# Optimization experiments

Hardware: AMD Instinct MI355X
Metric: run time of the kernel (lower is better)

The kernel has to match this reference:

```python
import jax, jax.numpy as jnp
import numpy as np

N = 8_000_000
THETA_W = 1.9  # physics-loss weight in forward()
EPS_DPDT = 1e-12
# Fixed config: bulk_modulus_model='tangent' (non-const), air_dissolution_model='on', air_fraction>0


def _drho_mix_dp(p, rho_L_atm, beta_L_atm, beta_gain, air_fraction, rho_g_atm,
                 polytropic_index, p_atm, p_crit, p_min):
    # mixture_density_derivative, vectorized over p (shape [N,1])
    p_used = jnp.maximum(p, p_min)
    L = p_crit - p_atm
    x = (p_used - p_atm) / L
    theta_mid = 1.0 - 3.0 * x**2 + 2.0 * x**3           # smoothstep between p_atm and p_crit
    theta = jnp.where(p_used <= p_atm, 1.0,
                      jnp.where(p_used >= p_crit, 0.0, theta_mid))
    dtheta_mid = 6.0 * (p_used - p_atm) * (p_used - p_crit) / L**3
    dtheta_dp = jnp.where((p_used <= p_atm) | (p_used >= p_crit), 0.0, dtheta_mid)

    afr = air_fraction / (1.0 - air_fraction)
    pr = (p_atm / p_used) ** (1.0 / polytropic_index)
    p_denom = afr * pr * theta
    p_ratio = afr * pr * (theta / (p_used * polytropic_index) - dtheta_dp)

    base = 1.0 + beta_gain * (p_used - p_atm) / beta_L_atm
    exp_term = base ** (-1.0 - 1.0 / beta_gain) / beta_L_atm

    rho_mix_init = rho_L_atm + rho_g_atm * afr
    denom = beta_L_atm * exp_term * base + p_denom
    return rho_mix_init * (exp_term + p_ratio) / denom**2


def setup_inputs() -> dict:
    key = jax.random.key(0)
    k1, k2, k3, k4 = jax.random.split(key, 4)
    outputs_P = jax.random.uniform(k1, (N, 1), dtype=jnp.float32) * 50.0  # p = 0.1*outputs_P in [0,5) MPa
    targets_P = outputs_P + 0.1 * jax.random.normal(k2, (N, 1), dtype=jnp.float32)
    dpdt = 0.5 * jax.random.normal(k3, (N, 1), dtype=jnp.float32)
    mdot_A = 0.01 * jax.random.normal(k4, (N, 1), dtype=jnp.float32)
    return {
        "targets_P": targets_P,
        "dpdt": dpdt,
        "mdot_A": mdot_A,
        "V": jnp.float32(1e-3),
        "outputs_P": outputs_P,
        "rho_L_atm": jnp.float32(850.0),
        "beta_L_atm": jnp.float32(1500.0),   # MPa
        "beta_gain": jnp.float32(10.0),
        "air_fraction": jnp.float32(0.005),
        "rho_g_atm": jnp.float32(1.2),
        "polytropic_index": jnp.float32(1.4),
        "p_atm": jnp.float32(0.101325),       # MPa
        "p_crit": jnp.float32(3.0),           # MPa
        "p_min": jnp.float32(0.01),           # MPa
    }


def reference(targets_P, dpdt, mdot_A, V, outputs_P, rho_L_atm, beta_L_atm,
              beta_gain, air_fraction, rho_g_atm, polytropic_index, p_atm,
              p_crit, p_min):
    drho = _drho_mix_dp(outputs_P * 0.1, rho_L_atm, beta_L_atm, beta_gain,
                        air_fraction, rho_g_atm, polytropic_index,
                        p_atm, p_crit, p_min)                      # [N,1]
    loss_physics = jnp.abs(V * drho * dpdt - mdot_A)                # [N,1]
    loss_M = jnp.abs(outputs_P - targets_P)                         # [N,1]
    per_sample = loss_M + THETA_W * loss_physics
    mask = jnp.abs(dpdt) >= EPS_DPDT                                # skip ~zero dpdt samples
    return jnp.sum(jnp.where(mask, per_sample, 0.0))
```

## Files before the change

### kernel.cpp

```cpp
#include <hip/hip_runtime.h>

#define THREADS 256
#define BLOCKS  2048

struct Consts {
    float p_min, p_atm, p_crit;
    float invL;
    float c_dth;
    float afr;
    float inv_n;
    float bg_over_bL;
    float inv_bL;
    float rho_mix_init;
    float V;
    float log2_patm;
    float pc1, pc2, pc3, pc4;
};

__device__ __forceinline__ float pow1p(float u, const Consts& c) {
    return fmaf(u, fmaf(u, fmaf(u, fmaf(u, c.pc4, c.pc3), c.pc2), c.pc1), 1.0f);
}

__device__ __forceinline__ float loss_elem(float oP, float tP, float dp, float md,
                                           const Consts& c) {
    float p  = 0.1f * oP;
    float pu = fmaxf(p, c.p_min);
    float dpa = pu - c.p_atm;
    float x = dpa * c.invL;
    float theta_mid = fmaf(x * x, fmaf(2.0f, x, -3.0f), 1.0f);
    bool lo = (pu <= c.p_atm);
    bool hi = (pu >= c.p_crit);
    float theta  = lo ? 1.0f : (hi ? 0.0f : theta_mid);
    float dtheta = (lo || hi) ? 0.0f : c.c_dth * dpa * (pu - c.p_crit);

    float inv_pu = __builtin_amdgcn_rcpf(pu);
    float lg_pu = __builtin_amdgcn_logf(pu);
    float pr = __builtin_amdgcn_exp2f(c.inv_n * (c.log2_patm - lg_pu));
    float apr = c.afr * pr;
    float p_denom = apr * theta;
    float p_ratio = apr * fmaf(theta * c.inv_n, inv_pu, -dtheta);

    float u  = dpa * c.bg_over_bL;
    float pb = pow1p(u, c);
    float exp_term = pb * c.inv_bL;
    float denom = fmaf(pb, u, pb) + p_denom;
    float inv_denom = __builtin_amdgcn_rcpf(denom);
    float drho = c.rho_mix_init * (exp_term + p_ratio) * inv_denom * inv_denom;

    float lp = fabsf(fmaf(c.V * dp, drho, -md));
    float lm = fabsf(oP - tP);
    float res = fmaf(1.9f, lp, lm);
    return (fabsf(dp) >= 1e-12f) ? res : 0.0f;
}

__global__ __launch_bounds__(THREADS) void loss_partial_kernel(
    const float* __restrict__ targets_P,
    const float* __restrict__ dpdt,
    const float* __restrict__ mdot_A,
    const float* __restrict__ outputs_P,
    const float* __restrict__ sV,
    const float* __restrict__ s_rhoL,
    const float* __restrict__ s_betaL,
    const float* __restrict__ s_bgain,
    const float* __restrict__ s_airfr,
    const float* __restrict__ s_rhog,
    const float* __restrict__ s_poly,
    const float* __restrict__ s_patm,
    const float* __restrict__ s_pcrit,
    const float* __restrict__ s_pmin,
    float* __restrict__ partials,
    int n)
{
    Consts c;
    {
        float beta_L = *s_betaL;
        float bgain  = *s_bgain;
        float airfr  = *s_airfr;
        float poly   = *s_poly;
        float patm   = *s_patm;
        float pcrit  = *s_pcrit;
        float L = pcrit - patm;
        c.p_min = *s_pmin;
        c.p_atm = patm;
        c.p_crit = pcrit;
        c.invL = 1.0f / L;
        c.c_dth = 6.0f / (L * L * L);
        c.afr = airfr / (1.0f - airfr);
        c.inv_n = 1.0f / poly;
        c.bg_over_bL = bgain / beta_L;
        c.inv_bL = 1.0f / beta_L;
        c.rho_mix_init = fmaf(*s_rhog, c.afr, *s_rhoL);
        c.V = *sV;
        c.log2_patm = __builtin_amdgcn_logf(patm);
        float a = -1.0f - 1.0f / bgain;
        c.pc1 = a;
        c.pc2 = a * (a - 1.0f) * 0.5f;
        c.pc3 = c.pc2 * (a - 2.0f) * (1.0f / 3.0f);
        c.pc4 = c.pc3 * (a - 3.0f) * 0.25f;
    }

    const int tid = blockIdx.x * blockDim.x + threadIdx.x;
    const int stride = gridDim.x * blockDim.x;
    const int n4 = n >> 2;

    const float4* o4 = (const float4*)outputs_P;
    const float4* t4 = (const float4*)targets_P;
    const float4* d4 = (const float4*)dpdt;
    const float4* m4 = (const float4*)mdot_A;

    float acc0 = 0.0f, acc1 = 0.0f;
    int i = tid;
    for (; i + stride < n4; i += 2 * stride) {
        float4 oa = o4[i];          float4 ob = o4[i + stride];
        float4 ta = t4[i];          float4 tb = t4[i + stride];
        float4 da = d4[i];          float4 db = d4[i + stride];
        float4 ma = m4[i];          float4 mb = m4[i + stride];
        acc0 += loss_elem(oa.x, ta.x, da.x, ma.x, c);
        acc1 += loss_elem(ob.x, tb.x, db.x, mb.x, c);
        acc0 += loss_elem(oa.y, ta.y, da.y, ma.y, c);
        acc1 += loss_elem(ob.y, tb.y, db.y, mb.y, c);
        acc0 += loss_elem(oa.z, ta.z, da.z, ma.z, c);
        acc1 += loss_elem(ob.z, tb.z, db.z, mb.z, c);
        acc0 += loss_elem(oa.w, ta.w, da.w, ma.w, c);
        acc1 += loss_elem(ob.w, tb.w, db.w, mb.w, c);
    }
    for (; i < n4; i += stride) {
        float4 o = o4[i];
        float4 t = t4[i];
        float4 d = d4[i];
        float4 m = m4[i];
        acc0 += loss_elem(o.x, t.x, d.x, m.x, c);
        acc1 += loss_elem(o.y, t.y, d.y, m.y, c);
        acc0 += loss_elem(o.z, t.z, d.z, m.z, c);
        acc1 += loss_elem(o.w, t.w, d.w, m.w, c);
    }
    for (int j = (n4 << 2) + tid; j < n; j += stride) {
        acc0 += loss_elem(outputs_P[j], targets_P[j], dpdt[j], mdot_A[j], c);
    }

    float acc = acc0 + acc1;
    for (int off = 32; off > 0; off >>= 1)
        acc += __shfl_down(acc, off, 64);
    __shared__ float wsum[THREADS / 64];
    int lane = threadIdx.x & 63, wid = threadIdx.x >> 6;
    if (lane == 0) wsum[wid] = acc;
    __syncthreads();
    if (threadIdx.x == 0) {
        float s = 0.0f;
        #pragma unroll
        for (int w = 0; w < THREADS / 64; ++w) s += wsum[w];
        partials[blockIdx.x] = s;
    }
}

__global__ __launch_bounds__(256) void loss_final_kernel(
    const float* __restrict__ partials, float* __restrict__ out, int nparts)
{
    double acc = 0.0;
    for (int i = threadIdx.x; i < nparts; i += blockDim.x)
        acc += (double)partials[i];
    for (int off = 32; off > 0; off >>= 1)
        acc += __shfl_down(acc, off, 64);
    __shared__ double wsum[4];
    int lane = threadIdx.x & 63, wid = threadIdx.x >> 6;
    if (lane == 0) wsum[wid] = acc;
    __syncthreads();
    if (threadIdx.x == 0) {
        double s = 0.0;
        #pragma unroll
        for (int w = 0; w < 4; ++w) s += wsum[w];
        out[0] = (float)s;
    }
}

extern "C" void kernel_launch(void* const* d_in, const int* in_sizes, int n_in,
                              void* d_out, int out_size, void* d_ws, size_t ws_size,
                              hipStream_t stream) {
    const float* targets_P = (const float*)d_in[0];
    const float* dpdt      = (const float*)d_in[1];
    const float* mdot_A    = (const float*)d_in[2];
    const float* sV        = (const float*)d_in[3];
    const float* outputs_P = (const float*)d_in[4];
    const float* s_rhoL    = (const float*)d_in[5];
    const float* s_betaL   = (const float*)d_in[6];
    const float* s_bgain   = (const float*)d_in[7];
    const float* s_airfr   = (const float*)d_in[8];
    const float* s_rhog    = (const float*)d_in[9];
    const float* s_poly    = (const float*)d_in[10];
    const float* s_patm    = (const float*)d_in[11];
    const float* s_pcrit   = (const float*)d_in[12];
    const float* s_pmin    = (const float*)d_in[13];

    int n = in_sizes[0];
    float* partials = (float*)d_ws;

    loss_partial_kernel<<<BLOCKS, THREADS, 0, stream>>>(
        targets_P, dpdt, mdot_A, outputs_P,
        sV, s_rhoL, s_betaL, s_bgain, s_airfr, s_rhog, s_poly,
        s_patm, s_pcrit, s_pmin,
        partials, n);

    loss_final_kernel<<<1, 256, 0, stream>>>(partials, (float*)d_out, BLOCKS);
}
```

Measured before the change: 167.3 us.

## Replace grid-stride loop with one float4 per thread and issue loads first

The persistent grid-stride kernel (2048 blocks) becomes a one-shot kernel where each thread handles a single float4 of each input, with the four vector loads issued before the per-block constant setup. The aim is to put the maximum number of memory requests in flight and hide the constant-setup latency behind the loads. In exchange it launches about 7800 blocks, each doing a block reduction and writing a partial, so the single-block final reduction has roughly four times more partials to sum. Out-of-range threads load a clamped index and are zero-weighted.

```diff
diff --git a/kernel.cpp b/kernel.cpp
--- a/kernel.cpp
+++ b/kernel.cpp
@@ -1,7 +1,6 @@
 #include <hip/hip_runtime.h>
 
 #define THREADS 256
-#define BLOCKS  2048
 
 struct Consts {
     float p_min, p_atm, p_crit;
@@ -53,7 +52,7 @@
     return (fabsf(dp) >= 1e-12f) ? res : 0.0f;
 }
 
-__global__ __launch_bounds__(THREADS) void loss_partial_kernel(
+__global__ __launch_bounds__(THREADS) void loss_kernel(
     const float* __restrict__ targets_P,
     const float* __restrict__ dpdt,
     const float* __restrict__ mdot_A,
@@ -71,6 +70,16 @@
     float* __restrict__ partials,
     int n)
 {
+    const int n4  = n >> 2;
+    const int idx = blockIdx.x * THREADS + threadIdx.x;
+    const bool valid = idx < n4;
+    const int s = valid ? idx : (n4 > 0 ? n4 - 1 : 0);
+
+    const float4 o = ((const float4*)outputs_P)[s];
+    const float4 t = ((const float4*)targets_P)[s];
+    const float4 d = ((const float4*)dpdt)[s];
+    const float4 m = ((const float4*)mdot_A)[s];
+
     Consts c;
     {
         float beta_L = *s_betaL;
@@ -99,46 +108,19 @@
         c.pc4 = c.pc3 * (a - 3.0f) * 0.25f;
     }
 
-    const int tid = blockIdx.x * blockDim.x + threadIdx.x;
-    const int stride = gridDim.x * blockDim.x;
-    const int n4 = n >> 2;
+    float w = valid ? 1.0f : 0.0f;
+    float sum = loss_elem(o.x, t.x, d.x, m.x, c)
+              + loss_elem(o.y, t.y, d.y, m.y, c)
+              + loss_elem(o.z, t.z, d.z, m.z, c)
+              + loss_elem(o.w, t.w, d.w, m.w, c);
+    float acc = w * sum;
 
-    const float4* o4 = (const float4*)outputs_P;
-    const float4* t4 = (const float4*)targets_P;
-    const float4* d4 = (const float4*)dpdt;
-    const float4* m4 = (const float4*)mdot_A;
-
-    float acc0 = 0.0f, acc1 = 0.0f;
-    int i = tid;
-    for (; i + stride < n4; i += 2 * stride) {
-        float4 oa = o4[i];          float4 ob = o4[i + stride];
-        float4 ta = t4[i];          float4 tb = t4[i + stride];
-        float4 da = d4[i];          float4 db = d4[i + stride];
-        float4 ma = m4[i];          float4 mb = m4[i + stride];
-        acc0 += loss_elem(oa.x, ta.x, da.x, ma.x, c);
-        acc1 += loss_elem(ob.x, tb.x, db.x, mb.x, c);
-        acc0 += loss_elem(oa.y, ta.y, da.y, ma.y, c);
-        acc1 += loss_elem(ob.y, tb.y, db.y, mb.y, c);
-        acc0 += loss_elem(oa.z, ta.z, da.z, ma.z, c);
-        acc1 += loss_elem(ob.z, tb.z, db.z, mb.z, c);
-        acc0 += loss_elem(oa.w, ta.w, da.w, ma.w, c);
-        acc1 += loss_elem(ob.w, tb.w, db.w, mb.w, c);
-    }
-    for (; i < n4; i += stride) {
-        float4 o = o4[i];
-        float4 t = t4[i];
-        float4 d = d4[i];
-        float4 m = m4[i];
-        acc0 += loss_elem(o.x, t.x, d.x, m.x, c);
-        acc1 += loss_elem(o.y, t.y, d.y, m.y, c);
-        acc0 += loss_elem(o.z, t.z, d.z, m.z, c);
-        acc1 += loss_elem(o.w, t.w, d.w, m.w, c);
-    }
-    for (int j = (n4 << 2) + tid; j < n; j += stride) {
-        acc0 += loss_elem(outputs_P[j], targets_P[j], dpdt[j], mdot_A[j], c);
+    if (blockIdx.x == 0) {
+        int j = (n4 << 2) + threadIdx.x;
+        if (j < n)
+            acc += loss_elem(outputs_P[j], targets_P[j], dpdt[j], mdot_A[j], c);
     }
 
-    float acc = acc0 + acc1;
     for (int off = 32; off > 0; off >>= 1)
         acc += __shfl_down(acc, off, 64);
     __shared__ float wsum[THREADS / 64];
@@ -146,10 +128,10 @@
     if (lane == 0) wsum[wid] = acc;
     __syncthreads();
     if (threadIdx.x == 0) {
-        float s = 0.0f;
+        float bsum = 0.0f;
         #pragma unroll
-        for (int w = 0; w < THREADS / 64; ++w) s += wsum[w];
-        partials[blockIdx.x] = s;
+        for (int v = 0; v < THREADS / 64; ++v) bsum += wsum[v];
+        partials[blockIdx.x] = bsum;
     }
 }
 
@@ -191,14 +173,18 @@
     const float* s_pcrit   = (const float*)d_in[12];
     const float* s_pmin    = (const float*)d_in[13];
 
-    int n = in_sizes[0];
+    int n  = in_sizes[0];
+    int n4 = n >> 2;
+    int nblocks = (n4 + THREADS - 1) / THREADS;
+    if (nblocks < 1) nblocks = 1;
+
     float* partials = (float*)d_ws;
 
-    loss_partial_kernel<<<BLOCKS, THREADS, 0, stream>>>(
+    loss_kernel<<<nblocks, THREADS, 0, stream>>>(
         targets_P, dpdt, mdot_A, outputs_P,
         sV, s_rhoL, s_betaL, s_bgain, s_airfr, s_rhog, s_poly,
         s_patm, s_pcrit, s_pmin,
         partials, n);
 
-    loss_final_kernel<<<1, 256, 0, stream>>>(partials, (float*)d_out, BLOCKS);
+    loss_final_kernel<<<1, 256, 0, stream>>>(partials, (float*)d_out, nblocks);
 }
```

After: 173.5 us. 3.7% more time.
